# Kernel tuning notes

Hardware: AMD Instinct MI355X
Metric: run time of the kernel (lower is better)

The kernel has to match this reference:

```python
import jax, jax.numpy as jnp
import numpy as np


def setup_inputs() -> dict:
    H = 512
    N, L = 64, 512
    key = jax.random.key(0)
    ks = jax.random.split(key, 9)
    s = 1.0 / np.sqrt(2 * H)  # torch Linear default init scale
    inp = {"x": jax.random.normal(ks[0], (N, L, H), dtype=jnp.float32)}
    names = ["f", "i", "o", "h"]
    for j, nm in enumerate(names):
        inp[f"W_{nm}"] = jax.random.uniform(ks[1 + 2 * j], (H, 2 * H), dtype=jnp.float32, minval=-s, maxval=s)
        inp[f"b_{nm}"] = jax.random.uniform(ks[2 + 2 * j], (H,), dtype=jnp.float32, minval=-s, maxval=s)
    return inp


def reference(x, W_f, b_f, W_i, b_i, W_o, b_o, W_h, b_h):
    N, L, H = x.shape
    # Fuse the 4 gate projections into one GEMM per step: W_all (4H, 2H)
    W_all = jnp.concatenate([W_f, W_i, W_o, W_h], axis=0)   # (4H, 2H)
    b_all = jnp.concatenate([b_f, b_i, b_o, b_h], axis=0)   # (4H,)
    # Precompute the input-half contribution for all timesteps at once:
    # concat([short, now]) @ W_all.T = short @ W_short.T + now @ W_now.T
    W_short, W_now = W_all[:, :H], W_all[:, H:]
    x_proj = jnp.einsum('nlh,gh->lng', x, W_now) + b_all     # (L, N, 4H)

    def step(carry, xp):
        long, short = carry                                   # each (N, H)
        gates = xp + short @ W_short.T                        # (N, 4H)
        f = jax.nn.sigmoid(gates[:, 0 * H:1 * H])
        i = jax.nn.sigmoid(gates[:, 1 * H:2 * H])
        o = jax.nn.sigmoid(gates[:, 2 * H:3 * H])
        h = gates[:, 3 * H:4 * H]                             # NOTE: no tanh (faithful to source)
        long = f * long + i * h
        short = o * jnp.tanh(long)
        return (long, short), short

    zeros = jnp.zeros((N, H), dtype=x.dtype)
    _, memories = jax.lax.scan(step, (zeros, zeros), x_proj)  # (L, N, H)
    return jnp.transpose(memories, (1, 0, 2))                 # (N, L, H)
```

## Files before the change

kernel.cpp:

```cpp
#include <hip/hip_runtime.h>
#include <stdint.h>

typedef short short8 __attribute__((ext_vector_type(8)));
typedef float float4v __attribute__((ext_vector_type(4)));
typedef uint32_t u32;
typedef uint64_t u64;

#define NSTEPS 512

__device__ __forceinline__ unsigned short f2bf(float f) {
  unsigned u = __builtin_bit_cast(unsigned, f);
  u += 0x7fffu + ((u >> 16) & 1u);
  return (unsigned short)(u >> 16);
}

__global__ __launch_bounds__(256) void xprep_kernel(const float* __restrict__ x,
                                                    short* __restrict__ xbf) {
  unsigned tid = blockIdx.x * 256u + threadIdx.x;
  unsigned lane = tid & 63u;
  unsigned kk   = (tid >> 6) & 15u;
  unsigned g    = (tid >> 10) & 3u;
  unsigned l    = tid >> 12;
  unsigned m = lane & 15u, qo = lane >> 4;
  const float* src = x + (((size_t)(g * 16u + m) * 512u + l) * 512u + kk * 32u + qo * 8u);
  float4 a  = ((const float4*)src)[0];
  float4 b2 = ((const float4*)src)[1];
  short8 v;
  v[0] = (short)f2bf(a.x);  v[1] = (short)f2bf(a.y);
  v[2] = (short)f2bf(a.z);  v[3] = (short)f2bf(a.w);
  v[4] = (short)f2bf(b2.x); v[5] = (short)f2bf(b2.y);
  v[6] = (short)f2bf(b2.z); v[7] = (short)f2bf(b2.w);
  *(short8*)(xbf + (size_t)tid * 8u) = v;
}

__global__ __launch_bounds__(256, 1) void lstm_persist(
    const float* __restrict__ Wfp, const float* __restrict__ bfp,
    const float* __restrict__ Wip, const float* __restrict__ bip,
    const float* __restrict__ Wop, const float* __restrict__ bop,
    const float* __restrict__ Whp, const float* __restrict__ bhp,
    const short* __restrict__ xbf,
    short* __restrict__ sbuf,
    u32* __restrict__ arrive,
    float* __restrict__ out)
{
  __shared__ float gl[4 * 16 * 17];

  const unsigned b = blockIdx.x;
  const unsigned g = (b & 7u) >> 1;
  const unsigned c = ((b >> 3) << 1) | (b & 1u);
  const unsigned t = threadIdx.x;
  const unsigned w = t >> 6;
  const unsigned lane = t & 63u;
  const unsigned m = lane & 15u, qo = lane >> 4;

  const float* Wsrc = (w == 0) ? Wfp : (w == 1) ? Wip : (w == 2) ? Wop : Whp;
  const float* bsrc = (w == 0) ? bfp : (w == 1) ? bip : (w == 2) ? bop : bhp;

  short8 wsf[16], wnf[16];
  {
    const float* wrow = Wsrc + (size_t)(c * 16u + m) * 1024u + qo * 8u;
#pragma unroll
    for (int kk = 0; kk < 16; kk++) {
      const float* p = wrow + kk * 32;
      short8 vs, vn;
#pragma unroll
      for (int j = 0; j < 8; j++) {
        vs[j] = (short)f2bf(p[j]);
        vn[j] = (short)f2bf(p[512 + j]);
      }
      wsf[kk] = vs;
      wnf[kk] = vn;
    }
  }
  const float bias = bsrc[c * 16u + m];

  const unsigned mm = t >> 4, hh = t & 15u;
  float longv = 0.f;
  float* outp = out + (size_t)(g * 16u + mm) * (512u * 512u) + (c * 16u + hh);

  u32* sdst;
  {
    unsigned k   = c * 16u + hh;
    unsigned kk2 = k >> 5;
    unsigned lw  = ((k >> 3) & 3u) * 16u + mm;
    unsigned jj  = k & 7u;
    sdst = (u32*)sbuf + ((((size_t)g) * 16u + kk2) * 64u + lw) * 4u + (jj >> 1);
  }
  const size_t sslot = (size_t)4u * 16u * 64u * 4u;

  const u32* fl = arrive + g * 32u;

  for (int l = 0; l < NSTEPS; l++) {
    const short8* xt = (const short8*)xbf + ((size_t)(l * 4 + g) * 16u) * 64u + lane;
    short8 xa[16];
#pragma unroll
    for (int kk = 0; kk < 16; kk++) xa[kk] = xt[(size_t)kk * 64u];

    float4v acc[4];
    {
      float4v bb = {bias, bias, bias, bias};
      float4v zz = {0.f, 0.f, 0.f, 0.f};
      acc[0] = bb; acc[1] = zz; acc[2] = zz; acc[3] = zz;
    }
#pragma unroll
    for (int kk = 0; kk < 16; kk++)
      acc[kk & 3] = __builtin_amdgcn_mfma_f32_16x16x32_bf16(xa[kk], wnf[kk], acc[kk & 3], 0, 0, 0);

    if (l > 0) {
      if (lane < 32u) {
        long spins = 0;
        while (__hip_atomic_load(fl + lane, __ATOMIC_RELAXED,
                                 __HIP_MEMORY_SCOPE_AGENT) < (u32)l) {
          __builtin_amdgcn_s_sleep(1);
          if (++spins > (100LL * 1000 * 1000)) break;
        }
      }

      const u64* st = (const u64*)sbuf +
                      ((size_t)(((unsigned)(l - 1) & 1u) * 4u + g) * 16u) * 64u * 2u +
                      (size_t)lane * 2u;
      u64 tmp[32];
#pragma unroll
      for (int kk = 0; kk < 16; kk++) {
        tmp[2 * kk]     = __hip_atomic_load(st + (size_t)kk * 128u, __ATOMIC_RELAXED,
                                            __HIP_MEMORY_SCOPE_AGENT);
        tmp[2 * kk + 1] = __hip_atomic_load(st + (size_t)kk * 128u + 1u, __ATOMIC_RELAXED,
                                            __HIP_MEMORY_SCOPE_AGENT);
      }
#pragma unroll
      for (int kk = 0; kk < 16; kk++) {
        struct { u64 a, b; } p = { tmp[2 * kk], tmp[2 * kk + 1] };
        short8 sa = __builtin_bit_cast(short8, p);
        acc[kk & 3] = __builtin_amdgcn_mfma_f32_16x16x32_bf16(sa, wsf[kk], acc[kk & 3], 0, 0, 0);
      }
    }

    float4v tot = (acc[0] + acc[1]) + (acc[2] + acc[3]);
#pragma unroll
    for (int r = 0; r < 4; r++)
      gl[(w * 16u + qo * 4u + (unsigned)r) * 17u + m] = tot[r];
    __syncthreads();

    float fg = gl[(0 * 16 + mm) * 17 + hh];
    float ig = gl[(1 * 16 + mm) * 17 + hh];
    float og = gl[(2 * 16 + mm) * 17 + hh];
    float hg = gl[(3 * 16 + mm) * 17 + hh];
    fg = 1.f / (1.f + __expf(-fg));
    ig = 1.f / (1.f + __expf(-ig));
    og = 1.f / (1.f + __expf(-og));
    longv = fg * longv + ig * hg;
    float e  = __expf(-2.f * fabsf(longv));
    float th = (1.f - e) / (1.f + e);
    th = (longv < 0.f) ? -th : th;
    float sh = og * th;

    unsigned short mybf = f2bf(sh);
    float shn = __shfl_xor(sh, 1);
    if ((t & 1u) == 0u) {
      u32 val = (u32)mybf | ((u32)f2bf(shn) << 16);
      __hip_atomic_store(sdst + ((size_t)((unsigned)l & 1u)) * sslot, val,
                         __ATOMIC_RELAXED, __HIP_MEMORY_SCOPE_AGENT);
    }
    __syncthreads();
    if (t == 0)
      __hip_atomic_store((u32*)(arrive + g * 32u + c), (u32)(l + 1),
                         __ATOMIC_RELAXED, __HIP_MEMORY_SCOPE_AGENT);

    outp[(size_t)l * 512u] = sh;
  }
}

extern "C" void kernel_launch(void* const* d_in, const int* in_sizes, int n_in,
                              void* d_out, int out_size, void* d_ws, size_t ws_size,
                              hipStream_t stream) {
  const float* x   = (const float*)d_in[0];
  const float* Wf  = (const float*)d_in[1];
  const float* bfv = (const float*)d_in[2];
  const float* Wi  = (const float*)d_in[3];
  const float* biv = (const float*)d_in[4];
  const float* Wo  = (const float*)d_in[5];
  const float* bov = (const float*)d_in[6];
  const float* Wh  = (const float*)d_in[7];
  const float* bhv = (const float*)d_in[8];
  float* out = (float*)d_out;

  char* ws = (char*)d_ws;
  short* xbf    = (short*)ws;
  short* sbuf   = (short*)(ws + 33554432);
  u32*   arrive = (u32*)(ws + 33554432 + 131072);

  hipMemsetAsync(ws + 33554432 + 131072, 0, 512, stream);

  xprep_kernel<<<8192, 256, 0, stream>>>(x, xbf);

  lstm_persist<<<128, 256, 0, stream>>>(Wf, bfv, Wi, biv, Wo, bov, Wh, bhv,
                                        xbf, sbuf, arrive, out);
}
```

Baseline: 2.102 ms.

## Replace per-step arrival flags with sentinel-valued data polling on full-history buffer

Instead of spinning on per-block arrival counters and then loading the hidden state, each step writes its bf16 state into a per-timestep slot of a 32MB buffer pre-filled with a sentinel pattern. Consumers load the data directly and re-poll until no word equals the sentinel, which removes the flag round-trip and the __syncthreads before the flag store. This costs a 32MB memset per launch, and a real value could in principle collide with the sentinel. The old flag path is kept as a fallback when the workspace is too small.

```diff
diff --git a/kernel.cpp b/kernel.cpp
--- a/kernel.cpp
+++ b/kernel.cpp
@@ -7,6 +7,7 @@
 typedef uint64_t u64;
 
 #define NSTEPS 512
+#define SENT 0x7F7F7F7Fu
 
 __device__ __forceinline__ unsigned short f2bf(float f) {
   unsigned u = __builtin_bit_cast(unsigned, f);
@@ -33,14 +34,13 @@
   *(short8*)(xbf + (size_t)tid * 8u) = v;
 }
 
-__global__ __launch_bounds__(256, 1) void lstm_persist(
+__global__ __launch_bounds__(256, 1) void lstm_persist_sent(
     const float* __restrict__ Wfp, const float* __restrict__ bfp,
     const float* __restrict__ Wip, const float* __restrict__ bip,
     const float* __restrict__ Wop, const float* __restrict__ bop,
     const float* __restrict__ Whp, const float* __restrict__ bhp,
     const short* __restrict__ xbf,
     short* __restrict__ sbuf,
-    u32* __restrict__ arrive,
     float* __restrict__ out)
 {
   __shared__ float gl[4 * 16 * 17];
@@ -84,11 +84,9 @@
     unsigned kk2 = k >> 5;
     unsigned lw  = ((k >> 3) & 3u) * 16u + mm;
     unsigned jj  = k & 7u;
-    sdst = (u32*)sbuf + ((((size_t)g) * 16u + kk2) * 64u + lw) * 4u + (jj >> 1);
-  }
-  const size_t sslot = (size_t)4u * 16u * 64u * 4u;
-
-  const u32* fl = arrive + g * 32u;
+    sdst = (u32*)sbuf + (((size_t)g * 16u + kk2) * 64u + lw) * 4u + (jj >> 1);
+  }
+  const size_t sslot_u32 = (size_t)4u * 16u * 64u * 4u;
 
   for (int l = 0; l < NSTEPS; l++) {
     const short8* xt = (const short8*)xbf + ((size_t)(l * 4 + g) * 16u) * 64u + lane;
@@ -107,29 +105,32 @@
       acc[kk & 3] = __builtin_amdgcn_mfma_f32_16x16x32_bf16(xa[kk], wnf[kk], acc[kk & 3], 0, 0, 0);
 
     if (l > 0) {
-      if (lane < 32u) {
+      const u64* st = (const u64*)sbuf +
+                      ((size_t)((unsigned)(l - 1) * 4u + g) * 16u) * 128u +
+                      (size_t)lane * 2u;
+      u64 lo[16], hi[16];
+#pragma unroll
+      for (int kk = 0; kk < 16; kk++) {
+        lo[kk] = __hip_atomic_load(st + (size_t)kk * 128u, __ATOMIC_RELAXED,
+                                   __HIP_MEMORY_SCOPE_AGENT);
+        hi[kk] = __hip_atomic_load(st + (size_t)kk * 128u + 1u, __ATOMIC_RELAXED,
+                                   __HIP_MEMORY_SCOPE_AGENT);
+      }
+#pragma unroll
+      for (int kk = 0; kk < 16; kk++) {
         long spins = 0;
-        while (__hip_atomic_load(fl + lane, __ATOMIC_RELAXED,
-                                 __HIP_MEMORY_SCOPE_AGENT) < (u32)l) {
-          __builtin_amdgcn_s_sleep(1);
-          if (++spins > (100LL * 1000 * 1000)) break;
+        for (;;) {
+          u64 a = lo[kk], b2 = hi[kk];
+          bool ok = ((u32)a != SENT) && ((u32)(a >> 32) != SENT) &&
+                    ((u32)b2 != SENT) && ((u32)(b2 >> 32) != SENT);
+          if (__all(ok)) break;
+          if (++spins > (50LL * 1000 * 1000)) break;
+          lo[kk] = __hip_atomic_load(st + (size_t)kk * 128u, __ATOMIC_RELAXED,
+                                     __HIP_MEMORY_SCOPE_AGENT);
+          hi[kk] = __hip_atomic_load(st + (size_t)kk * 128u + 1u, __ATOMIC_RELAXED,
+                                     __HIP_MEMORY_SCOPE_AGENT);
         }
-      }
-
-      const u64* st = (const u64*)sbuf +
-                      ((size_t)(((unsigned)(l - 1) & 1u) * 4u + g) * 16u) * 64u * 2u +
-                      (size_t)lane * 2u;
-      u64 tmp[32];
-#pragma unroll
-      for (int kk = 0; kk < 16; kk++) {
-        tmp[2 * kk]     = __hip_atomic_load(st + (size_t)kk * 128u, __ATOMIC_RELAXED,
-                                            __HIP_MEMORY_SCOPE_AGENT);
-        tmp[2 * kk + 1] = __hip_atomic_load(st + (size_t)kk * 128u + 1u, __ATOMIC_RELAXED,
-                                            __HIP_MEMORY_SCOPE_AGENT);
-      }
-#pragma unroll
-      for (int kk = 0; kk < 16; kk++) {
-        struct { u64 a, b; } p = { tmp[2 * kk], tmp[2 * kk + 1] };
+        struct { u64 a, b; } p = { lo[kk], hi[kk] };
         short8 sa = __builtin_bit_cast(short8, p);
         acc[kk & 3] = __builtin_amdgcn_mfma_f32_16x16x32_bf16(sa, wsf[kk], acc[kk & 3], 0, 0, 0);
       }
@@ -158,6 +159,109 @@
     float shn = __shfl_xor(sh, 1);
     if ((t & 1u) == 0u) {
       u32 val = (u32)mybf | ((u32)f2bf(shn) << 16);
+      __hip_atomic_store(sdst + (size_t)l * sslot_u32, val,
+                         __ATOMIC_RELAXED, __HIP_MEMORY_SCOPE_AGENT);
+    }
+    outp[(size_t)l * 512u] = sh;
+  }
+}
+
+__global__ __launch_bounds__(256, 1) void lstm_persist_flags(
+    const float* __restrict__ Wfp, const float* __restrict__ bfp,
+    const float* __restrict__ Wip, const float* __restrict__ bip,
+    const float* __restrict__ Wop, const float* __restrict__ bop,
+    const float* __restrict__ Whp, const float* __restrict__ bhp,
+    const short* __restrict__ xbf,
+    short* __restrict__ sbuf, u32* __restrict__ arrive,
+    float* __restrict__ out)
+{
+  __shared__ float gl[4 * 16 * 17];
+  const unsigned b = blockIdx.x;
+  const unsigned g = (b & 7u) >> 1;
+  const unsigned c = ((b >> 3) << 1) | (b & 1u);
+  const unsigned t = threadIdx.x;
+  const unsigned w = t >> 6;
+  const unsigned lane = t & 63u;
+  const unsigned m = lane & 15u, qo = lane >> 4;
+  const float* Wsrc = (w == 0) ? Wfp : (w == 1) ? Wip : (w == 2) ? Wop : Whp;
+  const float* bsrc = (w == 0) ? bfp : (w == 1) ? bip : (w == 2) ? bop : bhp;
+  short8 wsf[16], wnf[16];
+  {
+    const float* wrow = Wsrc + (size_t)(c * 16u + m) * 1024u + qo * 8u;
+#pragma unroll
+    for (int kk = 0; kk < 16; kk++) {
+      const float* p = wrow + kk * 32;
+      short8 vs, vn;
+#pragma unroll
+      for (int j = 0; j < 8; j++) { vs[j] = (short)f2bf(p[j]); vn[j] = (short)f2bf(p[512 + j]); }
+      wsf[kk] = vs; wnf[kk] = vn;
+    }
+  }
+  const float bias = bsrc[c * 16u + m];
+  const unsigned mm = t >> 4, hh = t & 15u;
+  float longv = 0.f;
+  float* outp = out + (size_t)(g * 16u + mm) * (512u * 512u) + (c * 16u + hh);
+  u32* sdst;
+  {
+    unsigned k = c * 16u + hh, kk2 = k >> 5, lw = ((k >> 3) & 3u) * 16u + mm, jj = k & 7u;
+    sdst = (u32*)sbuf + (((size_t)g * 16u + kk2) * 64u + lw) * 4u + (jj >> 1);
+  }
+  const size_t sslot = (size_t)4u * 16u * 64u * 4u;
+  const u32* fl = arrive + g * 32u;
+  for (int l = 0; l < NSTEPS; l++) {
+    const short8* xt = (const short8*)xbf + ((size_t)(l * 4 + g) * 16u) * 64u + lane;
+    short8 xa[16];
+#pragma unroll
+    for (int kk = 0; kk < 16; kk++) xa[kk] = xt[(size_t)kk * 64u];
+    float4v acc[4];
+    { float4v bb = {bias, bias, bias, bias}; float4v zz = {0.f, 0.f, 0.f, 0.f};
+      acc[0] = bb; acc[1] = zz; acc[2] = zz; acc[3] = zz; }
+#pragma unroll
+    for (int kk = 0; kk < 16; kk++)
+      acc[kk & 3] = __builtin_amdgcn_mfma_f32_16x16x32_bf16(xa[kk], wnf[kk], acc[kk & 3], 0, 0, 0);
+    if (l > 0) {
+      if (lane < 32u) {
+        long spins = 0;
+        while (__hip_atomic_load(fl + lane, __ATOMIC_RELAXED, __HIP_MEMORY_SCOPE_AGENT) < (u32)l) {
+          __builtin_amdgcn_s_sleep(1);
+          if (++spins > (100LL * 1000 * 1000)) break;
+        }
+      }
+      const u64* st = (const u64*)sbuf +
+                      ((size_t)(((unsigned)(l - 1) & 1u) * 4u + g) * 16u) * 128u + (size_t)lane * 2u;
+      u64 tmp[32];
+#pragma unroll
+      for (int kk = 0; kk < 16; kk++) {
+        tmp[2 * kk]     = __hip_atomic_load(st + (size_t)kk * 128u, __ATOMIC_RELAXED, __HIP_MEMORY_SCOPE_AGENT);
+        tmp[2 * kk + 1] = __hip_atomic_load(st + (size_t)kk * 128u + 1u, __ATOMIC_RELAXED, __HIP_MEMORY_SCOPE_AGENT);
+      }
+#pragma unroll
+      for (int kk = 0; kk < 16; kk++) {
+        struct { u64 a, b; } p = { tmp[2 * kk], tmp[2 * kk + 1] };
+        short8 sa = __builtin_bit_cast(short8, p);
+        acc[kk & 3] = __builtin_amdgcn_mfma_f32_16x16x32_bf16(sa, wsf[kk], acc[kk & 3], 0, 0, 0);
+      }
+    }
+    float4v tot = (acc[0] + acc[1]) + (acc[2] + acc[3]);
+#pragma unroll
+    for (int r = 0; r < 4; r++) gl[(w * 16u + qo * 4u + (unsigned)r) * 17u + m] = tot[r];
+    __syncthreads();
+    float fg = gl[(0 * 16 + mm) * 17 + hh];
+    float ig = gl[(1 * 16 + mm) * 17 + hh];
+    float og = gl[(2 * 16 + mm) * 17 + hh];
+    float hg = gl[(3 * 16 + mm) * 17 + hh];
+    fg = 1.f / (1.f + __expf(-fg));
+    ig = 1.f / (1.f + __expf(-ig));
+    og = 1.f / (1.f + __expf(-og));
+    longv = fg * longv + ig * hg;
+    float e = __expf(-2.f * fabsf(longv));
+    float th = (1.f - e) / (1.f + e);
+    th = (longv < 0.f) ? -th : th;
+    float sh = og * th;
+    unsigned short mybf = f2bf(sh);
+    float shn = __shfl_xor(sh, 1);
+    if ((t & 1u) == 0u) {
+      u32 val = (u32)mybf | ((u32)f2bf(shn) << 16);
       __hip_atomic_store(sdst + ((size_t)((unsigned)l & 1u)) * sslot, val,
                          __ATOMIC_RELAXED, __HIP_MEMORY_SCOPE_AGENT);
     }
@@ -165,7 +269,6 @@
     if (t == 0)
       __hip_atomic_store((u32*)(arrive + g * 32u + c), (u32)(l + 1),
                          __ATOMIC_RELAXED, __HIP_MEMORY_SCOPE_AGENT);
-
     outp[(size_t)l * 512u] = sh;
   }
 }
@@ -185,14 +288,23 @@
   float* out = (float*)d_out;
 
   char* ws = (char*)d_ws;
-  short* xbf    = (short*)ws;
-  short* sbuf   = (short*)(ws + 33554432);
-  u32*   arrive = (u32*)(ws + 33554432 + 131072);
-
-  hipMemsetAsync(ws + 33554432 + 131072, 0, 512, stream);
-
-  xprep_kernel<<<8192, 256, 0, stream>>>(x, xbf);
-
-  lstm_persist<<<128, 256, 0, stream>>>(Wf, bfv, Wi, biv, Wo, bov, Wh, bhv,
-                                        xbf, sbuf, arrive, out);
-}
+  short* xbf = (short*)ws;
+
+  const size_t XBF = 33554432;
+  const size_t SENT_BYTES = 33554432;
+
+  if (ws_size >= XBF + SENT_BYTES) {
+    short* sbuf = (short*)(ws + XBF);
+    hipMemsetAsync(ws + XBF, 0x7F, SENT_BYTES, stream);
+    xprep_kernel<<<8192, 256, 0, stream>>>(x, xbf);
+    lstm_persist_sent<<<128, 256, 0, stream>>>(Wf, bfv, Wi, biv, Wo, bov,
+                                               Wh, bhv, xbf, sbuf, out);
+  } else {
+    short* sbuf   = (short*)(ws + XBF);
+    u32*   arrive = (u32*)(ws + XBF + 131072);
+    hipMemsetAsync(ws + XBF + 131072, 0, 512, stream);
+    xprep_kernel<<<8192, 256, 0, stream>>>(x, xbf);
+    lstm_persist_flags<<<128, 256, 0, stream>>>(Wf, bfv, Wi, biv, Wo, bov,
+                                                Wh, bhv, xbf, sbuf, arrive, out);
+  }
+}
```

Result: slower. 2.454 ms (+16.8%).
